# Optimization experiments

Hardware: AMD Instinct MI355X
Metric: run time of the kernel (lower is better)

Reference implementation:

```python
import jax, jax.numpy as jnp
import numpy as np

N_NODES = 100000
NUM_FEAT = 64
NUM_CLASS = 40
N_EDGES = 1600000


def setup_inputs() -> dict:
    key = jax.random.key(0)
    k1, k2, k3, k4, k5 = jax.random.split(key, 5)
    x = jax.random.normal(k1, (N_NODES, NUM_FEAT), dtype=jnp.float32)
    index = jax.random.randint(k2, (2, N_EDGES), 0, N_NODES, dtype=jnp.int64)
    # SAGEConv params: lin_l applied to aggregated neighbors (has bias),
    # lin_r applied to root features (no bias) -- PyG convention.
    s = 1.0 / np.sqrt(NUM_FEAT)
    lin_l_w = jax.random.uniform(k3, (NUM_FEAT, NUM_CLASS), dtype=jnp.float32, minval=-s, maxval=s)
    lin_l_b = jnp.zeros((NUM_CLASS,), dtype=jnp.float32)
    lin_r_w = jax.random.uniform(k4, (NUM_FEAT, NUM_CLASS), dtype=jnp.float32, minval=-s, maxval=s)
    return {"x": x, "index": index, "lin_l_w": lin_l_w, "lin_l_b": lin_l_b, "lin_r_w": lin_r_w}


def reference(x, index, lin_l_w, lin_l_b, lin_r_w):
    src, dst = index[0], index[1]
    # Mean aggregation over incoming neighbors: messages flow src -> dst.
    msg = x[src]                                        # [E, F] gather
    agg_sum = jax.ops.segment_sum(msg, dst, num_segments=N_NODES)   # [N, F]
    deg = jax.ops.segment_sum(jnp.ones((index.shape[1],), dtype=x.dtype), dst,
                              num_segments=N_NODES)     # [N]
    agg = agg_sum / jnp.maximum(deg, 1.0)[:, None]      # mean, safe for isolated nodes
    out = agg @ lin_l_w + lin_l_b + x @ lin_r_w         # [N, C]
    return jax.nn.log_softmax(out, axis=1)
```

## Files before the change

### kernel.cpp

```cpp
#include <hip/hip_runtime.h>
#include <hip/hip_fp8.h>
#include <math.h>

constexpr int NODES = 100000;
constexpr int F = 64;
constexpr int C = 40;
constexpr int NPB   = 128;
constexpr int NB    = (NODES + NPB - 1) / NPB;
constexpr int NBPAD = 1024;
constexpr int BCAP  = 2816;
constexpr int TILE  = 4096;
constexpr int NTILES = NODES / 16;
constexpr int MBLK  = (NTILES + 3) / 4;

typedef __attribute__((ext_vector_type(8))) short short8;
typedef __attribute__((ext_vector_type(4))) float floatx4;
typedef __attribute__((ext_vector_type(2))) float floatx2;

__device__ inline unsigned bf16pack2(float a, float b) {
    unsigned ua = __builtin_bit_cast(unsigned, a);
    unsigned ub = __builtin_bit_cast(unsigned, b);
    ua += 0x7FFFu + ((ua >> 16) & 1u);
    ub += 0x7FFFu + ((ub >> 16) & 1u);
    return (ua >> 16) | (ub & 0xFFFF0000u);
}
__device__ inline unsigned short bf16of(float a) {
    unsigned ua = __builtin_bit_cast(unsigned, a);
    ua += 0x7FFFu + ((ua >> 16) & 1u);
    return (unsigned short)(ua >> 16);
}
__device__ inline float bf16tof(unsigned short u) {
    return __builtin_bit_cast(float, (unsigned)u << 16);
}
__device__ inline unsigned char fp8of(float f) {
    __hip_fp8_e4m3 q(f);
    return (unsigned char)q.__x;
}
template <int K>
__device__ inline float fp8byte(unsigned d) {
    __hip_fp8_e4m3 v;
    v.__x = (__hip_fp8_storage_t)((d >> (8 * K)) & 0xFFu);
    return (float)v;
}
template <int HI>
__device__ inline floatx2 fp8pk(unsigned d) {
#if __has_builtin(__builtin_amdgcn_cvt_pk_f32_fp8)
    return __builtin_amdgcn_cvt_pk_f32_fp8((int)d, HI != 0);
#else
    floatx2 r;
    r[0] = fp8byte<HI ? 2 : 0>(d);
    r[1] = fp8byte<HI ? 3 : 1>(d);
    return r;
#endif
}

__global__ __launch_bounds__(256)
void fused_A(const float* __restrict__ x,
             const float* __restrict__ wl,
             const float* __restrict__ bl,
             const float* __restrict__ wr,
             const int* __restrict__ src, const int* __restrict__ dst,
             int* __restrict__ gcursor, int* __restrict__ bbuf, int nedges,
             unsigned char* __restrict__ y8f, unsigned short* __restrict__ z8) {
    __shared__ union {
        struct { int lhist[NB]; int lcur[NB]; } bz;
        struct { unsigned sB[10 * 64 * 4]; float sbl[40]; } mf;
    } sh;

    int t = threadIdx.x;

    if (blockIdx.x < MBLK) {
        if (t < 40) sh.mf.sbl[t] = bl[t];
        for (int s = t; s < 640; s += 256) {
            int region = s >> 6;
            int l      = s & 63;
            int ct = region >> 1, ks = region & 1;
            int col = ct * 16 + (l & 15);
            int fb  = ks * 32 + ((l >> 4) << 3);
            const float* wsrc = (col < 40) ? (wl + col) : (wr + (col - 40));
            unsigned* dstp = &sh.mf.sB[s * 4];
#pragma unroll
            for (int p = 0; p < 4; ++p) {
                float a = wsrc[(fb + 2 * p) * 40];
                float b = wsrc[(fb + 2 * p + 1) * 40];
                dstp[p] = bf16pack2(a, b);
            }
        }
        __syncthreads();

        int lane = t & 63;
        int nt = blockIdx.x * 4 + (t >> 6);
        if (nt >= NTILES) return;

        union U { unsigned u[4]; short8 v; };
        short8 bf[5][2];
#pragma unroll
        for (int ct = 0; ct < 5; ++ct)
#pragma unroll
            for (int ks = 0; ks < 2; ++ks) {
                U tmp;
                const uint4* p =
                    (const uint4*)&sh.mf.sB[((ct * 2 + ks) * 64 + lane) * 4];
                uint4 q = *p;
                tmp.u[0] = q.x; tmp.u[1] = q.y; tmp.u[2] = q.z; tmp.u[3] = q.w;
                bf[ct][ks] = tmp.v;
            }

        floatx4 acc[5];
#pragma unroll
        for (int ct = 0; ct < 5; ++ct) {
            int col = ct * 16 + (lane & 15);
            float bias = (col >= 40) ? sh.mf.sbl[col - 40] : 0.0f;
            acc[ct] = (floatx4){bias, bias, bias, bias};
        }

        int row = nt * 16 + (lane & 15);
        const float4* xp = (const float4*)(x + (size_t)row * F);
        short8 af[2];
#pragma unroll
        for (int ks = 0; ks < 2; ++ks) {
            int kb = ks * 8 + ((lane >> 4) << 1);
            float4 va = xp[kb];
            float4 vb = xp[kb + 1];
            U a;
            a.u[0] = bf16pack2(va.x, va.y);
            a.u[1] = bf16pack2(va.z, va.w);
            a.u[2] = bf16pack2(vb.x, vb.y);
            a.u[3] = bf16pack2(vb.z, vb.w);
            af[ks] = a.v;
        }

#pragma unroll
        for (int ks = 0; ks < 2; ++ks)
#pragma unroll
            for (int ct = 0; ct < 5; ++ct)
                acc[ct] = __builtin_amdgcn_mfma_f32_16x16x32_bf16(
                    af[ks], bf[ct][ks], acc[ct], 0, 0, 0);

#pragma unroll
        for (int ct = 0; ct < 5; ++ct) {
            int col = ct * 16 + (lane & 15);
#pragma unroll
            for (int r = 0; r < 4; ++r) {
                int grow = nt * 16 + ((lane >> 4) << 2) + r;
                if (col < 40) y8f[(size_t)grow * C + col]       = fp8of(acc[ct][r]);
                else          z8[(size_t)grow * C + (col - 40)] = bf16of(acc[ct][r]);
            }
        }
    } else {
        for (int i = t; i < NB; i += 256) sh.bz.lhist[i] = 0;
        __syncthreads();

        int bb = blockIdx.x - MBLK;
        int base = bb * TILE;
        int pk[16], bk[16];
#pragma unroll
        for (int u = 0; u < 16; ++u) {
            int e = base + u * 256 + t;
            bk[u] = -1;
            if (e < nedges) {
                int s = src[e], d = dst[e];
                if ((unsigned)s < (unsigned)NODES && (unsigned)d < (unsigned)NODES) {
                    bk[u] = d >> 7;
                    pk[u] = s | ((d & 127) << 17);
                    atomicAdd(&sh.bz.lhist[bk[u]], 1);
                }
            }
        }
        __syncthreads();
        for (int i = t; i < NB; i += 256) {
            int c = sh.bz.lhist[i];
            sh.bz.lcur[i] = c ? atomicAdd(&gcursor[i], c) : 0;
        }
        __syncthreads();
#pragma unroll
        for (int u = 0; u < 16; ++u) {
            if (bk[u] >= 0) {
                int p = atomicAdd(&sh.bz.lcur[bk[u]], 1);
                if (p < BCAP) bbuf[(size_t)bk[u] * BCAP + p] = pk[u];
            }
        }
    }
}

__global__ __launch_bounds__(256)
void local_sort(const int* __restrict__ bbuf, const int* __restrict__ gcount,
                int* __restrict__ sorted_src, int* __restrict__ off,
                int* __restrict__ deg) {
    __shared__ int lhist[NPB];
    __shared__ int lcur[NPB];
    __shared__ int wred[4];
    __shared__ int w0tot;

    int b = blockIdx.x;
    int t = threadIdx.x;
    int lane = t & 63, wv = t >> 6;

    int part = 0;
    for (int i = t; i < b; i += 256) part += gcount[i];
#pragma unroll
    for (int d = 1; d < 64; d <<= 1) part += __shfl_xor(part, d);
    if (lane == 0) wred[wv] = part;
    if (t < NPB) lhist[t] = 0;
    __syncthreads();
    int ebase = wred[0] + wred[1] + wred[2] + wred[3];

    int cnt = gcount[b];
    if (cnt > BCAP) cnt = BCAP;
    const int* myb = bbuf + (size_t)b * BCAP;

    for (int i = t; i < cnt; i += 256)
        atomicAdd(&lhist[myb[i] >> 17], 1);
    __syncthreads();

    int c = 0, sc = 0;
    if (t < NPB) {
        c = lhist[t];
        sc = c;
#pragma unroll
        for (int d = 1; d < 64; d <<= 1) {
            int o = __shfl_up(sc, d);
            if (lane >= d) sc += o;
        }
    }
    if (t == 63) w0tot = sc;
    __syncthreads();
    if (t >= 64 && t < NPB) sc += w0tot;
    if (t < NPB) {
        int excl = ebase + sc - c;
        lcur[t] = excl;
        int n = b * NPB + t;
        if (n < NODES) { off[n] = excl; deg[n] = c; }
    }
    __syncthreads();

    for (int i = t; i < cnt; i += 256) {
        int pk = myb[i];
        int p = atomicAdd(&lcur[pk >> 17], 1);
        sorted_src[p] = pk & 0x1FFFF;
    }
}

__global__ __launch_bounds__(256)
void aggregate_v4(const unsigned char* __restrict__ y8f,
                  const unsigned short* __restrict__ z8,
                  const int* __restrict__ sorted_src,
                  const int* __restrict__ off,
                  const int* __restrict__ deg,
                  float* __restrict__ out) {
    int t = threadIdx.x;
    int lane = t & 63;
    int n = blockIdx.x * 4 + (t >> 6);
    if (n >= NODES) return;

    int g = lane >> 3;
    int i = lane & 7;
    bool valid = (i < 5);
    int byteoff = (valid ? i : 4) * 8;

    int base = __builtin_amdgcn_readfirstlane(off[n]);
    int cnt  = __builtin_amdgcn_readfirstlane(deg[n]);

    int li = lane < cnt ? lane : (cnt > 0 ? cnt - 1 : 0);
    int idxv = sorted_src[base + li];

    uint4 zv = make_uint4(0u, 0u, 0u, 0u);
    if (valid) zv = *(const uint4*)(z8 + (size_t)n * C + i * 8);

    unsigned d0[8], d1[8];
#pragma unroll
    for (int k = 0; k < 8; ++k) { d0[k] = 0u; d1[k] = 0u; }
#pragma unroll
    for (int k = 0; k < 8; ++k) {
        if (cnt > 8 * k) {
            int s = __shfl(idxv, 8 * k + g);
            const unsigned* p = (const unsigned*)(y8f + (size_t)s * C + byteoff);
            d0[k] = p[0];
            d1[k] = p[1];
        }
    }

    float acc[8] = {0.f, 0.f, 0.f, 0.f, 0.f, 0.f, 0.f, 0.f};
#pragma unroll
    for (int k = 0; k < 8; ++k) {
        if (cnt > 8 * k) {
            float w = (8 * k + g < cnt) ? 1.0f : 0.0f;
            floatx2 l0 = fp8pk<0>(d0[k]);
            floatx2 h0 = fp8pk<1>(d0[k]);
            floatx2 l1 = fp8pk<0>(d1[k]);
            floatx2 h1 = fp8pk<1>(d1[k]);
            acc[0] = fmaf(w, l0[0], acc[0]);
            acc[1] = fmaf(w, l0[1], acc[1]);
            acc[2] = fmaf(w, h0[0], acc[2]);
            acc[3] = fmaf(w, h0[1], acc[3]);
            acc[4] = fmaf(w, l1[0], acc[4]);
            acc[5] = fmaf(w, l1[1], acc[5]);
            acc[6] = fmaf(w, h1[0], acc[6]);
            acc[7] = fmaf(w, h1[1], acc[7]);
        }
    }
    for (int j = 64; j < cnt; j += 8) {
        int e = j + g;
        int ec = e < cnt ? e : cnt - 1;
        int s = sorted_src[base + ec];
        float w = e < cnt ? 1.0f : 0.0f;
        const unsigned* p = (const unsigned*)(y8f + (size_t)s * C + byteoff);
        unsigned a0 = p[0], a1 = p[1];
        floatx2 l0 = fp8pk<0>(a0), h0 = fp8pk<1>(a0);
        floatx2 l1 = fp8pk<0>(a1), h1 = fp8pk<1>(a1);
        acc[0] = fmaf(w, l0[0], acc[0]);
        acc[1] = fmaf(w, l0[1], acc[1]);
        acc[2] = fmaf(w, h0[0], acc[2]);
        acc[3] = fmaf(w, h0[1], acc[3]);
        acc[4] = fmaf(w, l1[0], acc[4]);
        acc[5] = fmaf(w, l1[1], acc[5]);
        acc[6] = fmaf(w, h1[0], acc[6]);
        acc[7] = fmaf(w, h1[1], acc[7]);
    }

#pragma unroll
    for (int m = 8; m <= 32; m <<= 1)
#pragma unroll
        for (int k = 0; k < 8; ++k)
            acc[k] += __shfl_xor(acc[k], m);

    float inv = 1.0f / (float)(cnt > 0 ? cnt : 1);

    float o[8];
    if (valid) {
        unsigned zu[4] = {zv.x, zv.y, zv.z, zv.w};
#pragma unroll
        for (int k = 0; k < 4; ++k) {
            o[2 * k]     = bf16tof((unsigned short)(zu[k] & 0xFFFFu))
                         + acc[2 * k] * inv;
            o[2 * k + 1] = bf16tof((unsigned short)(zu[k] >> 16))
                         + acc[2 * k + 1] * inv;
        }
    } else {
#pragma unroll
        for (int k = 0; k < 8; ++k) o[k] = -1e30f;
    }

    float mv = -1e30f;
    if (valid)
#pragma unroll
        for (int k = 0; k < 8; ++k) mv = fmaxf(mv, o[k]);
#pragma unroll
    for (int m = 1; m <= 4; m <<= 1) mv = fmaxf(mv, __shfl_xor(mv, m));

    float ev = 0.0f;
    if (valid)
#pragma unroll
        for (int k = 0; k < 8; ++k) ev += __expf(o[k] - mv);
#pragma unroll
    for (int m = 1; m <= 4; m <<= 1) ev += __shfl_xor(ev, m);
    float lse = mv + __logf(ev);

    if (valid && g == 0) {
        float4 o0 = make_float4(o[0] - lse, o[1] - lse, o[2] - lse, o[3] - lse);
        float4 o1 = make_float4(o[4] - lse, o[5] - lse, o[6] - lse, o[7] - lse);
        float4* op = (float4*)(out + (size_t)n * C + i * 8);
        op[0] = o0;
        op[1] = o1;
    }
}

__global__ __launch_bounds__(256)
void scatter_kernel(const float* __restrict__ x, const int* __restrict__ src,
                    const int* __restrict__ dst, float* __restrict__ aggsum,
                    float* __restrict__ deg, int nedges) {
    int lane = threadIdx.x & 63;
    int e = blockIdx.x * 4 + (threadIdx.x >> 6);
    if (e >= nedges) return;
    int s = src[e], d = dst[e];
    if ((unsigned)s >= (unsigned)NODES || (unsigned)d >= (unsigned)NODES) return;
    atomicAdd(&aggsum[(size_t)d * F + lane], x[(size_t)s * F + lane]);
    if (lane == 0) atomicAdd(&deg[d], 1.0f);
}

__global__ __launch_bounds__(256)
void meanify_kernel(float* __restrict__ aggsum, const float* __restrict__ deg) {
    int lane = threadIdx.x & 63;
    int n = blockIdx.x * 4 + (threadIdx.x >> 6);
    if (n >= NODES) return;
    aggsum[(size_t)n * F + lane] *= 1.0f / fmaxf(deg[n], 1.0f);
}

__global__ __launch_bounds__(256)
void node_kernel(const float* __restrict__ x, const float* __restrict__ aggmean,
                 const float* __restrict__ wl, const float* __restrict__ bl,
                 const float* __restrict__ wr, float* __restrict__ out) {
    __shared__ alignas(16) float sWl[F * C];
    __shared__ alignas(16) float sWr[F * C];
    __shared__ alignas(16) float sb[C];
    for (int i = threadIdx.x; i < F * C; i += 256) { sWl[i] = wl[i]; sWr[i] = wr[i]; }
    if (threadIdx.x < C) sb[threadIdx.x] = bl[threadIdx.x];
    __syncthreads();
    int n = blockIdx.x * 256 + threadIdx.x;
    if (n >= NODES) return;
    float4 acc[10];
    const float4* sb4 = (const float4*)sb;
#pragma unroll
    for (int q = 0; q < 10; ++q) acc[q] = sb4[q];
    const float4* xr  = (const float4*)(x       + (size_t)n * F);
    const float4* ar  = (const float4*)(aggmean + (size_t)n * F);
    const float4* wl4 = (const float4*)sWl;
    const float4* wr4 = (const float4*)sWr;
    for (int f4 = 0; f4 < F / 4; ++f4) {
        float4 xv = xr[f4], av = ar[f4];
        float xs[4]  = {xv.x, xv.y, xv.z, xv.w};
        float as_[4] = {av.x, av.y, av.z, av.w};
#pragma unroll
        for (int jj = 0; jj < 4; ++jj) {
            int f = f4 * 4 + jj;
#pragma unroll
            for (int q = 0; q < 10; ++q) {
                float4 wlv = wl4[f * 10 + q], wrv = wr4[f * 10 + q];
                acc[q].x = fmaf(as_[jj], wlv.x, fmaf(xs[jj], wrv.x, acc[q].x));
                acc[q].y = fmaf(as_[jj], wlv.y, fmaf(xs[jj], wrv.y, acc[q].y));
                acc[q].z = fmaf(as_[jj], wlv.z, fmaf(xs[jj], wrv.z, acc[q].z));
                acc[q].w = fmaf(as_[jj], wlv.w, fmaf(xs[jj], wrv.w, acc[q].w));
            }
        }
    }
    float m = -1e30f;
#pragma unroll
    for (int q = 0; q < 10; ++q)
        m = fmaxf(m, fmaxf(fmaxf(acc[q].x, acc[q].y), fmaxf(acc[q].z, acc[q].w)));
    float ssum = 0.0f;
#pragma unroll
    for (int q = 0; q < 10; ++q)
        ssum += __expf(acc[q].x - m) + __expf(acc[q].y - m) +
                __expf(acc[q].z - m) + __expf(acc[q].w - m);
    float lse = m + __logf(ssum);
    float4* op = (float4*)(out + (size_t)n * C);
#pragma unroll
    for (int q = 0; q < 10; ++q) {
        float4 v;
        v.x = acc[q].x - lse; v.y = acc[q].y - lse;
        v.z = acc[q].z - lse; v.w = acc[q].w - lse;
        op[q] = v;
    }
}

extern "C" void kernel_launch(void* const* d_in, const int* in_sizes, int n_in,
                              void* d_out, int out_size, void* d_ws, size_t ws_size,
                              hipStream_t stream) {
    const float* x     = (const float*)d_in[0];
    const int*   index = (const int*)d_in[1];
    const float* wl    = (const float*)d_in[2];
    const float* bl    = (const float*)d_in[3];
    const float* wr    = (const float*)d_in[4];
    float* out = (float*)d_out;

    int nedges = in_sizes[1] / 2;
    const int* src = index;
    const int* dst = index + nedges;

    size_t need = (size_t)NODES * C * 3
                + ((size_t)NB * BCAP + (size_t)nedges + 2 * (size_t)NODES + NBPAD) * 4;

    if (ws_size >= need) {
        unsigned short* z8 = (unsigned short*)d_ws;
        unsigned char* y8f = (unsigned char*)(z8 + (size_t)NODES * C);
        int* bbuf       = (int*)(y8f + (size_t)NODES * C);
        int* sorted_src = bbuf + (size_t)NB * BCAP;
        int* off        = sorted_src + nedges;
        int* deg        = off + NODES;
        int* gcursor    = deg + NODES;

        hipMemsetAsync(gcursor, 0, NBPAD * sizeof(int), stream);

        int bblocks = (nedges + TILE - 1) / TILE;
        fused_A<<<MBLK + bblocks, 256, 0, stream>>>(
            x, wl, bl, wr, src, dst, gcursor, bbuf, nedges, y8f, z8);
        local_sort<<<NB, 256, 0, stream>>>(bbuf, gcursor, sorted_src, off, deg);
        aggregate_v4<<<(NODES + 3) / 4, 256, 0, stream>>>(
            y8f, z8, sorted_src, off, deg, out);
    } else {
        float* aggsum = (float*)d_ws;
        float* deg    = aggsum + (size_t)NODES * F;
        hipMemsetAsync(d_ws, 0,
                       ((size_t)NODES * F + NODES) * sizeof(float), stream);
        scatter_kernel<<<(nedges + 3) / 4, 256, 0, stream>>>(
            x, src, dst, aggsum, deg, nedges);
        meanify_kernel<<<(NODES + 3) / 4, 256, 0, stream>>>(aggsum, deg);
        node_kernel<<<(NODES + 255) / 256, 256, 0, stream>>>(
            x, aggsum, wl, bl, wr, out);
    }
}
```

Before: 166.2 us.

## Map eight nodes per wavefront in aggregation with sequential per-group neighbor loops

The aggregation kernel changes from one node per 64-lane wavefront to one node per 8-lane group, so each wave handles eight nodes. Each group walks its node's neighbor list serially, two edges per step, and prefetches the next pair of indices. This drops the cross-group shuffle reduction and the idle lanes that low-degree nodes left behind. In exchange, per-lane loop length now follows each node's own degree, so divergence within a wave grows, and each gather has fewer loads in flight.

```diff
diff --git a/kernel.cpp b/kernel.cpp
--- a/kernel.cpp
+++ b/kernel.cpp
@@ -241,8 +241,16 @@
     }
 }
 
-__global__ __launch_bounds__(256)
-void aggregate_v4(const unsigned char* __restrict__ y8f,
+__device__ inline void acc8(float (&acc)[8], uint2 q) {
+    floatx2 v;
+    v = fp8pk<0>(q.x); acc[0] += v[0]; acc[1] += v[1];
+    v = fp8pk<1>(q.x); acc[2] += v[0]; acc[3] += v[1];
+    v = fp8pk<0>(q.y); acc[4] += v[0]; acc[5] += v[1];
+    v = fp8pk<1>(q.y); acc[6] += v[0]; acc[7] += v[1];
+}
+
+__global__ __launch_bounds__(256)
+void aggregate_v5(const unsigned char* __restrict__ y8f,
                   const unsigned short* __restrict__ z8,
                   const int* __restrict__ sorted_src,
                   const int* __restrict__ off,
@@ -250,79 +258,45 @@
                   float* __restrict__ out) {
     int t = threadIdx.x;
     int lane = t & 63;
-    int n = blockIdx.x * 4 + (t >> 6);
-    if (n >= NODES) return;
-
+    int wv = t >> 6;
     int g = lane >> 3;
     int i = lane & 7;
+    int n = blockIdx.x * 32 + wv * 8 + g;
+    if (n >= NODES) return;
+
     bool valid = (i < 5);
     int byteoff = (valid ? i : 4) * 8;
 
-    int base = __builtin_amdgcn_readfirstlane(off[n]);
-    int cnt  = __builtin_amdgcn_readfirstlane(deg[n]);
-
-    int li = lane < cnt ? lane : (cnt > 0 ? cnt - 1 : 0);
-    int idxv = sorted_src[base + li];
+    int base = off[n];
+    int cnt  = deg[n];
 
     uint4 zv = make_uint4(0u, 0u, 0u, 0u);
     if (valid) zv = *(const uint4*)(z8 + (size_t)n * C + i * 8);
 
-    unsigned d0[8], d1[8];
-#pragma unroll
-    for (int k = 0; k < 8; ++k) { d0[k] = 0u; d1[k] = 0u; }
-#pragma unroll
-    for (int k = 0; k < 8; ++k) {
-        if (cnt > 8 * k) {
-            int s = __shfl(idxv, 8 * k + g);
-            const unsigned* p = (const unsigned*)(y8f + (size_t)s * C + byteoff);
-            d0[k] = p[0];
-            d1[k] = p[1];
-        }
-    }
-
     float acc[8] = {0.f, 0.f, 0.f, 0.f, 0.f, 0.f, 0.f, 0.f};
-#pragma unroll
-    for (int k = 0; k < 8; ++k) {
-        if (cnt > 8 * k) {
-            float w = (8 * k + g < cnt) ? 1.0f : 0.0f;
-            floatx2 l0 = fp8pk<0>(d0[k]);
-            floatx2 h0 = fp8pk<1>(d0[k]);
-            floatx2 l1 = fp8pk<0>(d1[k]);
-            floatx2 h1 = fp8pk<1>(d1[k]);
-            acc[0] = fmaf(w, l0[0], acc[0]);
-            acc[1] = fmaf(w, l0[1], acc[1]);
-            acc[2] = fmaf(w, h0[0], acc[2]);
-            acc[3] = fmaf(w, h0[1], acc[3]);
-            acc[4] = fmaf(w, l1[0], acc[4]);
-            acc[5] = fmaf(w, l1[1], acc[5]);
-            acc[6] = fmaf(w, h1[0], acc[6]);
-            acc[7] = fmaf(w, h1[1], acc[7]);
-        }
-    }
-    for (int j = 64; j < cnt; j += 8) {
-        int e = j + g;
-        int ec = e < cnt ? e : cnt - 1;
-        int s = sorted_src[base + ec];
-        float w = e < cnt ? 1.0f : 0.0f;
-        const unsigned* p = (const unsigned*)(y8f + (size_t)s * C + byteoff);
-        unsigned a0 = p[0], a1 = p[1];
-        floatx2 l0 = fp8pk<0>(a0), h0 = fp8pk<1>(a0);
-        floatx2 l1 = fp8pk<0>(a1), h1 = fp8pk<1>(a1);
-        acc[0] = fmaf(w, l0[0], acc[0]);
-        acc[1] = fmaf(w, l0[1], acc[1]);
-        acc[2] = fmaf(w, h0[0], acc[2]);
-        acc[3] = fmaf(w, h0[1], acc[3]);
-        acc[4] = fmaf(w, l1[0], acc[4]);
-        acc[5] = fmaf(w, l1[1], acc[5]);
-        acc[6] = fmaf(w, h1[0], acc[6]);
-        acc[7] = fmaf(w, h1[1], acc[7]);
-    }
-
-#pragma unroll
-    for (int m = 8; m <= 32; m <<= 1)
-#pragma unroll
-        for (int k = 0; k < 8; ++k)
-            acc[k] += __shfl_xor(acc[k], m);
+    const int* sp = sorted_src + base;
+
+    int npair = cnt >> 1;
+    if (npair > 0) {
+        int s0 = sp[0];
+        int s1 = sp[1];
+        for (int p = 0; p < npair; ++p) {
+            int c0 = s0, c1 = s1;
+            int nx = 2 * p + 2;
+            int pi = (nx + 1 < cnt) ? nx : cnt - 2;
+            s0 = sp[pi];
+            s1 = sp[pi + 1];
+            uint2 q0 = *(const uint2*)(y8f + (size_t)c0 * C + byteoff);
+            uint2 q1 = *(const uint2*)(y8f + (size_t)c1 * C + byteoff);
+            acc8(acc, q0);
+            acc8(acc, q1);
+        }
+    }
+    if (cnt & 1) {
+        int c = sp[cnt - 1];
+        uint2 q = *(const uint2*)(y8f + (size_t)c * C + byteoff);
+        acc8(acc, q);
+    }
 
     float inv = 1.0f / (float)(cnt > 0 ? cnt : 1);
 
@@ -356,7 +330,7 @@
     for (int m = 1; m <= 4; m <<= 1) ev += __shfl_xor(ev, m);
     float lse = mv + __logf(ev);
 
-    if (valid && g == 0) {
+    if (valid) {
         float4 o0 = make_float4(o[0] - lse, o[1] - lse, o[2] - lse, o[3] - lse);
         float4 o1 = make_float4(o[4] - lse, o[5] - lse, o[6] - lse, o[7] - lse);
         float4* op = (float4*)(out + (size_t)n * C + i * 8);
@@ -475,7 +449,7 @@
         fused_A<<<MBLK + bblocks, 256, 0, stream>>>(
             x, wl, bl, wr, src, dst, gcursor, bbuf, nedges, y8f, z8);
         local_sort<<<NB, 256, 0, stream>>>(bbuf, gcursor, sorted_src, off, deg);
-        aggregate_v4<<<(NODES + 3) / 4, 256, 0, stream>>>(
+        aggregate_v5<<<(NODES + 31) / 32, 256, 0, stream>>>(
             y8f, z8, sorted_src, off, deg, out);
     } else {
         float* aggsum = (float*)d_ws;
```

Result: faster. 150.8 us (-9.2%).
